# Performance work log

Hardware: AMD Instinct MI355X
Metric: run time of the kernel (lower is better)

## Reference

```python
import jax, jax.numpy as jnp
import numpy as np

N_STATE = 64   # S4 state size N
L_MAX = 4096   # sequence length
H = 256        # number of SSM channels (d_model)
BATCH = 16


def _green_roots(Lambda, P, B, C, step, L):
    """Frequency-domain S4 kernel at the L roots of unity (Q = P, DPLR).
    Lambda,P,B,C: complex[N]; step: scalar. Returns complex[L]."""
    Omega = jnp.exp(-2j * jnp.pi * (jnp.arange(L) / L))          # (L,)
    g = (2.0 / step) * ((1.0 - Omega) / (1.0 + Omega))           # (L,)
    c = 2.0 / (1.0 + Omega)                                      # (L,)
    # four Cauchy numerators stacked: k00,k01,k10,k11
    vs = jnp.stack([C.conj() * B, C.conj() * P,
                    P.conj() * B, P.conj() * P])                 # (4,N)
    denom = g[:, None] - Lambda[None, :]                         # (L,N)
    k = jnp.einsum('kn,ln->kl', vs, 1.0 / denom)                 # (4,L)
    k00, k01, k10, k11 = k
    return c * (k00 - k01 * (1.0 / (1.0 + k11)) * k10)           # (L,)


def _kernel_freq(Lambda_re, Lambda_im, P_re, P_im, B_re, B_im,
                 C_re, C_im, log_step, L):
    Lambda = (Lambda_re + 1j * Lambda_im).astype(jnp.complex64)  # (H,N)
    P = (P_re + 1j * P_im).astype(jnp.complex64)
    Bm = (B_re + 1j * B_im).astype(jnp.complex64)
    Cm = (C_re + 1j * C_im).astype(jnp.complex64)
    step = jnp.exp(log_step)                                     # (H,)
    f = lambda lam, p, b, c, s: _green_roots(lam, p, b, c, s, L)
    return jax.vmap(f)(Lambda, P, Bm, Cm, step)                  # (H,L)


def setup_inputs() -> dict:
    key = jax.random.key(0)
    ks = jax.random.split(key, 10)
    u = jax.random.normal(ks[0], (BATCH, H, L_MAX), dtype=jnp.float32)
    # stable continuous-time poles: negative real part, spread imag parts
    Lambda_re = -0.5 * jnp.ones((H, N_STATE), jnp.float32) \
        - jax.random.uniform(ks[1], (H, N_STATE), dtype=jnp.float32)
    Lambda_im = jnp.pi * jax.random.normal(ks[2], (H, N_STATE), dtype=jnp.float32) * N_STATE / 8
    scale = 1.0 / np.sqrt(N_STATE)
    P_re = scale * jax.random.normal(ks[3], (H, N_STATE), dtype=jnp.float32)
    P_im = scale * jax.random.normal(ks[4], (H, N_STATE), dtype=jnp.float32)
    B_re = scale * jax.random.normal(ks[5], (H, N_STATE), dtype=jnp.float32)
    B_im = scale * jax.random.normal(ks[6], (H, N_STATE), dtype=jnp.float32)
    C_re = scale * jax.random.normal(ks[7], (H, N_STATE), dtype=jnp.float32)
    C_im = scale * jax.random.normal(ks[8], (H, N_STATE), dtype=jnp.float32)
    # log-uniform step in [1e-3, 1e-1] (log_step_initializer)
    log_step = (jax.random.uniform(ks[9], (H,), dtype=jnp.float32)
                * (np.log(0.1) - np.log(0.001)) + np.log(0.001)).astype(jnp.float32)
    return {"u": u, "Lambda_re": Lambda_re, "Lambda_im": Lambda_im,
            "P_re": P_re, "P_im": P_im, "B_re": B_re, "B_im": B_im,
            "C_re": C_re, "C_im": C_im, "log_step": log_step}


def reference(u, Lambda_re, Lambda_im, P_re, P_im, B_re, B_im,
              C_re, C_im, log_step):
    L = u.shape[-1]
    Kf = _kernel_freq(Lambda_re, Lambda_im, P_re, P_im, B_re, B_im,
                      C_re, C_im, log_step, L)                   # (H,L) complex
    # circular_convolution_complex, batched over (BATCH,H)
    ud = jnp.fft.fft(u, axis=-1)                                  # (B,H,L)
    y = jnp.fft.ifft(ud * Kf[None, :, :], n=L, axis=-1)
    return y.real.astype(jnp.float32)                             # (B,H,L)
```

## Files before the change

### kernel.cpp

```cpp
#include <hip/hip_runtime.h>
#include <math.h>

#define NSTATE 64
#define LEN    4096
#define NH     256
#define NB     16

__device__ float2 g_ksym[NH * LEN];
__device__ float4 g_pA[NH * NSTATE];
__device__ float4 g_pB[NH * NSTATE];
__device__ float2 g_pC[NH * NSTATE];

__device__ __forceinline__ int rev8_12(int p) {
  return ((p & 7) << 9) | (((p >> 3) & 7) << 6) | (((p >> 6) & 7) << 3) | (p >> 9);
}

__device__ __forceinline__ float2 cadd(float2 a, float2 b){ return make_float2(a.x+b.x, a.y+b.y); }
__device__ __forceinline__ float2 csub(float2 a, float2 b){ return make_float2(a.x-b.x, a.y-b.y); }
__device__ __forceinline__ float2 cmul(float2 a, float2 b){ return make_float2(a.x*b.x - a.y*b.y, a.x*b.y + a.y*b.x); }
__device__ __forceinline__ float2 mulnegi(float2 a){ return make_float2(a.y, -a.x); }
__device__ __forceinline__ float2 mulposi(float2 a){ return make_float2(-a.y, a.x); }

#define RSQ2 0.70710678118654752f

__device__ __forceinline__ void bfly8_fwd(float2 v[8]) {
  float2 a0 = cadd(v[0], v[4]), b0 = csub(v[0], v[4]);
  float2 a1 = cadd(v[1], v[5]), d1 = csub(v[1], v[5]);
  float2 a2 = cadd(v[2], v[6]), d2 = csub(v[2], v[6]);
  float2 a3 = cadd(v[3], v[7]), d3 = csub(v[3], v[7]);
  float2 b1 = make_float2(RSQ2 * (d1.x + d1.y), RSQ2 * (d1.y - d1.x));
  float2 b2 = mulnegi(d2);
  float2 b3 = make_float2(RSQ2 * (d3.y - d3.x), -RSQ2 * (d3.x + d3.y));
  float2 u0 = cadd(a0, a2), u1 = csub(a0, a2), u2 = cadd(a1, a3), u3 = csub(a1, a3);
  v[0] = cadd(u0, u2);
  v[2] = cadd(u1, mulnegi(u3));
  v[4] = csub(u0, u2);
  v[6] = cadd(u1, mulposi(u3));
  float2 w0 = cadd(b0, b2), w1 = csub(b0, b2), w2 = cadd(b1, b3), w3 = csub(b1, b3);
  v[1] = cadd(w0, w2);
  v[3] = cadd(w1, mulnegi(w3));
  v[5] = csub(w0, w2);
  v[7] = cadd(w1, mulposi(w3));
}

__device__ __forceinline__ void bfly8_inv(float2 v[8]) {
  float2 a0 = cadd(v[0], v[4]), b0 = csub(v[0], v[4]);
  float2 a1 = cadd(v[1], v[5]), d1 = csub(v[1], v[5]);
  float2 a2 = cadd(v[2], v[6]), d2 = csub(v[2], v[6]);
  float2 a3 = cadd(v[3], v[7]), d3 = csub(v[3], v[7]);
  float2 b1 = make_float2(RSQ2 * (d1.x - d1.y), RSQ2 * (d1.x + d1.y));
  float2 b2 = mulposi(d2);
  float2 b3 = make_float2(-RSQ2 * (d3.x + d3.y), RSQ2 * (d3.x - d3.y));
  float2 u0 = cadd(a0, a2), u1 = csub(a0, a2), u2 = cadd(a1, a3), u3 = csub(a1, a3);
  v[0] = cadd(u0, u2);
  v[2] = cadd(u1, mulposi(u3));
  v[4] = csub(u0, u2);
  v[6] = cadd(u1, mulnegi(u3));
  float2 w0 = cadd(b0, b2), w1 = csub(b0, b2), w2 = cadd(b1, b3), w3 = csub(b1, b3);
  v[1] = cadd(w0, w2);
  v[3] = cadd(w1, mulposi(w3));
  v[5] = csub(w0, w2);
  v[7] = cadd(w1, mulnegi(w3));
}

__device__ __forceinline__ void twiddle7(float2 v[8], float wr, float wi) {
  float2 w1 = make_float2(wr, wi);
  float2 w2 = cmul(w1, w1);
  float2 w3 = cmul(w2, w1);
  float2 w4 = cmul(w2, w2);
  float2 w5 = cmul(w3, w2);
  float2 w6 = cmul(w3, w3);
  float2 w7 = cmul(w4, w3);
  v[1] = cmul(v[1], w1); v[2] = cmul(v[2], w2); v[3] = cmul(v[3], w3);
  v[4] = cmul(v[4], w4); v[5] = cmul(v[5], w5); v[6] = cmul(v[6], w6);
  v[7] = cmul(v[7], w7);
}

#define WAVE_SYNC() asm volatile("s_waitcnt lgkmcnt(0)" ::: "memory")

__global__ __launch_bounds__(256) void s4_prep(
    const float* __restrict__ Lre, const float* __restrict__ Lim,
    const float* __restrict__ Pre, const float* __restrict__ Pim,
    const float* __restrict__ Bre, const float* __restrict__ Bim,
    const float* __restrict__ Cre, const float* __restrict__ Cim)
{
  int idx = blockIdx.x * 256 + threadIdx.x;
  if (idx >= NH * NSTATE) return;
  float lr = Lre[idx], li = Lim[idx];
  float pr = Pre[idx], pi = Pim[idx];
  float br = Bre[idx], bi = Bim[idx];
  float cr = Cre[idx], ci = Cim[idx];
  g_pA[idx] = make_float4(lr, li, pr * pr + pi * pi, 0.0f);
  g_pB[idx] = make_float4(cr * br + ci * bi, cr * bi - ci * br,
                          cr * pr + ci * pi, cr * pi - ci * pr);
  g_pC[idx] = make_float2(pr * br + pi * bi, pr * bi - pi * br);
}

__global__ __launch_bounds__(256) void s4_kernel_freq(const float* __restrict__ log_step)
{
  const int b = blockIdx.x;
  const int h = b >> 2;
  const int q = ((b & 3) << 8) | threadIdx.x;
  const float step = expf(log_step[h]);
  const float ts = 2.0f / step;
  const float NEG2PI = -6.2831853071795864769f;

  float gar, gai, car, cai, gbr, gbi, cbr, cbi;
  float gcr, gci, ccr, cci, gdr, gdi, cdr, cdi;
  {
    float so, co;
    sincosf(NEG2PI * ((float)q * (1.0f / (float)LEN)), &so, &co);
    float dr = 1.0f + co, di = so;
    float inv = 1.0f / fmaf(dr, dr, di * di);
    car = 2.0f * dr * inv; cai = -2.0f * di * inv;
    float nr = 1.0f - co, ni = -so;
    gar = ts * (fmaf(nr, dr, ni * di) * inv);
    gai = ts * (fmaf(ni, dr, -nr * di) * inv);
  }
  if (q == 0) {
    float so, co;
    sincosf(NEG2PI * 0.5f, &so, &co);
    float dr = 1.0f + co, di = so;
    float inv = 1.0f / fmaf(dr, dr, di * di);
    cbr = 2.0f * dr * inv; cbi = -2.0f * di * inv;
    float nr = 1.0f - co, ni = -so;
    gbr = ts * (fmaf(nr, dr, ni * di) * inv);
    gbi = ts * (fmaf(ni, dr, -nr * di) * inv);
  } else {
    gbr = gar; gbi = -gai; cbr = car; cbi = -cai;
  }
  {
    float so, co;
    sincosf(NEG2PI * ((float)(q + 1024) * (1.0f / (float)LEN)), &so, &co);
    float dr = 1.0f + co, di = so;
    float inv = 1.0f / fmaf(dr, dr, di * di);
    ccr = 2.0f * dr * inv; cci = -2.0f * di * inv;
    float nr = 1.0f - co, ni = -so;
    gcr = ts * (fmaf(nr, dr, ni * di) * inv);
    gci = ts * (fmaf(ni, dr, -nr * di) * inv);
  }
  gdr = gcr; gdi = -gci; cdr = ccr; cdi = -cci;

  float A00r=0,A00i=0,A01r=0,A01i=0,A10r=0,A10i=0,A11r=0,A11i=0;
  float B00r=0,B00i=0,B01r=0,B01i=0,B10r=0,B10i=0,B11r=0,B11i=0;
  float C00r=0,C00i=0,C01r=0,C01i=0,C10r=0,C10i=0,C11r=0,C11i=0;
  float D00r=0,D00i=0,D01r=0,D01i=0,D10r=0,D10i=0,D11r=0,D11i=0;

  const float4* __restrict__ pa = g_pA + h * NSTATE;
  const float4* __restrict__ pb = g_pB + h * NSTATE;
  const float2* __restrict__ pc = g_pC + h * NSTATE;

#define CAUCHY(gre, gim, k00r,k00i,k01r,k01i,k10r,k10i,k11r,k11i)            \
  {                                                                          \
    float rd = gre - Av.x, id = gim - Av.y;                                  \
    float idn = __builtin_amdgcn_rcpf(fmaf(rd, rd, id * id));                \
    float ir = rd * idn, ii = -(id * idn);                                   \
    k00r = fmaf(Bv.x, ir, k00r); k00r = fmaf(-Bv.y, ii, k00r);               \
    k00i = fmaf(Bv.x, ii, k00i); k00i = fmaf(Bv.y, ir, k00i);                \
    k01r = fmaf(Bv.z, ir, k01r); k01r = fmaf(-Bv.w, ii, k01r);               \
    k01i = fmaf(Bv.z, ii, k01i); k01i = fmaf(Bv.w, ir, k01i);                \
    k10r = fmaf(Cv.x, ir, k10r); k10r = fmaf(-Cv.y, ii, k10r);               \
    k10i = fmaf(Cv.x, ii, k10i); k10i = fmaf(Cv.y, ir, k10i);                \
    k11r = fmaf(Av.z, ir, k11r); k11i = fmaf(Av.z, ii, k11i);                \
  }

#pragma unroll 4
  for (int n = 0; n < NSTATE; ++n) {
    float4 Av = pa[n];
    float4 Bv = pb[n];
    float2 Cv = pc[n];
    CAUCHY(gar, gai, A00r,A00i,A01r,A01i,A10r,A10i,A11r,A11i)
    CAUCHY(gbr, gbi, B00r,B00i,B01r,B01i,B10r,B10i,B11r,B11i)
    CAUCHY(gcr, gci, C00r,C00i,C01r,C01i,C10r,C10i,C11r,C11i)
    CAUCHY(gdr, gdi, D00r,D00i,D01r,D01i,D10r,D10i,D11r,D11i)
  }
#undef CAUCHY

#define FINISH(cr_, ci_, k00r,k00i,k01r,k01i,k10r,k10i,k11r,k11i, Kr, Ki)    \
  {                                                                          \
    float rr = 1.0f + k11r, ri = k11i;                                       \
    float rinv = 1.0f / fmaf(rr, rr, ri * ri);                               \
    float pr_ = k01r * k10r - k01i * k10i;                                   \
    float pi_ = k01r * k10i + k01i * k10r;                                   \
    float wr = (pr_ * rr + pi_ * ri) * rinv;                                 \
    float wi = (pi_ * rr - pr_ * ri) * rinv;                                 \
    float sr = k00r - wr, si = k00i - wi;                                    \
    Kr = cr_ * sr - ci_ * si; Ki = cr_ * si + ci_ * sr;                      \
  }

  float Kar, Kai, Kbr, Kbi, Kcr, Kci, Kdr, Kdi;
  FINISH(car, cai, A00r,A00i,A01r,A01i,A10r,A10i,A11r,A11i, Kar, Kai)
  FINISH(cbr, cbi, B00r,B00i,B01r,B01i,B10r,B10i,B11r,B11i, Kbr, Kbi)
  FINISH(ccr, cci, C00r,C00i,C01r,C01i,C10r,C10i,C11r,C11i, Kcr, Kci)
  FINISH(cdr, cdi, D00r,D00i,D01r,D01i,D10r,D10i,D11r,D11i, Kdr, Kdi)
#undef FINISH

  float2* out = g_ksym + (size_t)h * LEN;
  if (q == 0) {
    out[rev8_12(0)]    = make_float2(Kar, 0.0f);
    out[rev8_12(2048)] = make_float2(Kbr, 0.0f);
  } else {
    float fr = 0.5f * (Kar + Kbr), fi = 0.5f * (Kai - Kbi);
    out[rev8_12(q)]       = make_float2(fr, fi);
    out[rev8_12(LEN - q)] = make_float2(fr, -fi);
  }
  {
    float fr = 0.5f * (Kcr + Kdr), fi = 0.5f * (Kci - Kdi);
    out[rev8_12(1024 + q)] = make_float2(fr, fi);
    out[rev8_12(3072 - q)] = make_float2(fr, -fi);
  }
}

__global__ __launch_bounds__(512) void s4_fftconv(const float* __restrict__ u,
                                                 float* __restrict__ y)
{
  __shared__ float2 X[4608];

  const int t = threadIdx.x;
  const int bid = blockIdx.x;
  const int h  = bid & (NH - 1);
  const int bp = bid >> 8;

  const int w  = t >> 6;
  const int i  = t & 63;
  const int i3 = i >> 3;
  const int i7 = i & 7;
  const int R  = 576 * w;

  float c1, s1, c2, s2, c3, s3;
  sincosf((float)t  * (-6.2831853071795864769f / 4096.0f), &s1, &c1);
  sincosf((float)i  * (-6.2831853071795864769f /  512.0f), &s2, &c2);
  sincosf((float)i7 * (-6.2831853071795864769f /   64.0f), &s3, &c3);

  const float* u1 = u + ((size_t)bp * NH + h) * LEN;
  const float* u2 = u + ((size_t)(bp + 8) * NH + h) * LEN;

  float2 v[8];
#pragma unroll
  for (int m = 0; m < 8; ++m)
    v[m] = make_float2(u1[t + 512 * m], u2[t + 512 * m]);
  bfly8_fwd(v);
  twiddle7(v, c1, s1);
#pragma unroll
  for (int m = 0; m < 8; ++m) X[576 * m + t] = v[m];
  __syncthreads();

#pragma unroll
  for (int m = 0; m < 8; ++m) v[m] = X[R + i + 64 * m];
  bfly8_fwd(v);
  twiddle7(v, c2, s2);
#pragma unroll
  for (int m = 0; m < 8; ++m) X[R + 68 * m + i] = v[m];
  WAVE_SYNC();

#pragma unroll
  for (int m = 0; m < 8; ++m) v[m] = X[R + 68 * i3 + i7 + 8 * m];
  bfly8_fwd(v);
  twiddle7(v, c3, s3);
#pragma unroll
  for (int m = 0; m < 8; ++m) X[R + 9 * (8 * i3 + m) + i7] = v[m];
  WAVE_SYNC();

  {
    const float4* kp = (const float4*)(g_ksym + (size_t)h * LEN + 8 * t);
    float4 k0 = kp[0], k1 = kp[1], k2 = kp[2], k3 = kp[3];
#pragma unroll
    for (int m = 0; m < 8; ++m) v[m] = X[R + 9 * i + m];
    bfly8_fwd(v);
    v[0] = cmul(v[0], make_float2(k0.x, k0.y));
    v[1] = cmul(v[1], make_float2(k0.z, k0.w));
    v[2] = cmul(v[2], make_float2(k1.x, k1.y));
    v[3] = cmul(v[3], make_float2(k1.z, k1.w));
    v[4] = cmul(v[4], make_float2(k2.x, k2.y));
    v[5] = cmul(v[5], make_float2(k2.z, k2.w));
    v[6] = cmul(v[6], make_float2(k3.x, k3.y));
    v[7] = cmul(v[7], make_float2(k3.z, k3.w));
    bfly8_inv(v);
#pragma unroll
    for (int p = 0; p < 8; ++p) X[R + 9 * i + p] = v[p];
  }
  WAVE_SYNC();

#pragma unroll
  for (int m = 0; m < 8; ++m) v[m] = X[R + 9 * (8 * i3 + m) + i7];
  twiddle7(v, c3, -s3);
  bfly8_inv(v);
#pragma unroll
  for (int p = 0; p < 8; ++p) X[R + 68 * i3 + i7 + 8 * p] = v[p];
  WAVE_SYNC();

#pragma unroll
  for (int m = 0; m < 8; ++m) v[m] = X[R + 68 * m + i];
  twiddle7(v, c2, -s2);
  bfly8_inv(v);
#pragma unroll
  for (int p = 0; p < 8; ++p) X[R + i + 64 * p] = v[p];
  __syncthreads();

#pragma unroll
  for (int m = 0; m < 8; ++m) v[m] = X[576 * m + t];
  twiddle7(v, c1, -s1);
  bfly8_inv(v);

  float* y1 = y + ((size_t)bp * NH + h) * LEN;
  float* y2 = y + ((size_t)(bp + 8) * NH + h) * LEN;
  const float sc = 1.0f / (float)LEN;
#pragma unroll
  for (int p = 0; p < 8; ++p) {
    y1[t + 512 * p] = v[p].x * sc;
    y2[t + 512 * p] = v[p].y * sc;
  }
}

extern "C" void kernel_launch(void* const* d_in, const int* in_sizes, int n_in,
                              void* d_out, int out_size, void* d_ws, size_t ws_size,
                              hipStream_t stream) {
  const float* u    = (const float*)d_in[0];
  const float* Lre  = (const float*)d_in[1];
  const float* Lim  = (const float*)d_in[2];
  const float* Pre  = (const float*)d_in[3];
  const float* Pim  = (const float*)d_in[4];
  const float* Bre  = (const float*)d_in[5];
  const float* Bim  = (const float*)d_in[6];
  const float* Cre  = (const float*)d_in[7];
  const float* Cim  = (const float*)d_in[8];
  const float* lstep = (const float*)d_in[9];
  float* y = (float*)d_out;

  s4_prep<<<(NH * NSTATE + 255) / 256, 256, 0, stream>>>(Lre, Lim, Pre, Pim, Bre, Bim, Cre, Cim);
  s4_kernel_freq<<<NH * 4, 256, 0, stream>>>(lstep);
  s4_fftconv<<<NH * (NB / 2), 512, 0, stream>>>(u, y);
}
```

Baseline: 180.4 us.

## Fuse S4 prep into kernel-frequency kernel with shared-memory parameters and more blocks

Removes the separate prep kernel and computes the per-channel Cauchy numerators inside the frequency kernel, storing them in shared memory instead of global scratch arrays. Each thread now evaluates two conjugate frequency points instead of four, and the grid is doubled to NH*8 blocks, lowering register pressure and raising parallelism. The intent is to save one kernel launch and the global round trip. The cost is redundant prep work: each of the 8 blocks per channel recomputes the same 64 parameters, plus an added block barrier.

```diff
diff --git a/kernel.cpp b/kernel.cpp
--- a/kernel.cpp
+++ b/kernel.cpp
@@ -7,9 +7,6 @@
 #define NB     16
 
 __device__ float2 g_ksym[NH * LEN];
-__device__ float4 g_pA[NH * NSTATE];
-__device__ float4 g_pB[NH * NSTATE];
-__device__ float2 g_pC[NH * NSTATE];
 
 __device__ __forceinline__ int rev8_12(int p) {
   return ((p & 7) << 9) | (((p >> 3) & 7) << 6) | (((p >> 6) & 7) << 3) | (p >> 9);
@@ -78,38 +75,41 @@
 
 #define WAVE_SYNC() asm volatile("s_waitcnt lgkmcnt(0)" ::: "memory")
 
-__global__ __launch_bounds__(256) void s4_prep(
+__global__ __launch_bounds__(256) void s4_kernel_freq(
     const float* __restrict__ Lre, const float* __restrict__ Lim,
     const float* __restrict__ Pre, const float* __restrict__ Pim,
     const float* __restrict__ Bre, const float* __restrict__ Bim,
-    const float* __restrict__ Cre, const float* __restrict__ Cim)
+    const float* __restrict__ Cre, const float* __restrict__ Cim,
+    const float* __restrict__ log_step)
 {
-  int idx = blockIdx.x * 256 + threadIdx.x;
-  if (idx >= NH * NSTATE) return;
-  float lr = Lre[idx], li = Lim[idx];
-  float pr = Pre[idx], pi = Pim[idx];
-  float br = Bre[idx], bi = Bim[idx];
-  float cr = Cre[idx], ci = Cim[idx];
-  g_pA[idx] = make_float4(lr, li, pr * pr + pi * pi, 0.0f);
-  g_pB[idx] = make_float4(cr * br + ci * bi, cr * bi - ci * br,
-                          cr * pr + ci * pi, cr * pi - ci * pr);
-  g_pC[idx] = make_float2(pr * br + pi * bi, pr * bi - pi * br);
-}
-
-__global__ __launch_bounds__(256) void s4_kernel_freq(const float* __restrict__ log_step)
-{
-  const int b = blockIdx.x;
-  const int h = b >> 2;
-  const int q = ((b & 3) << 8) | threadIdx.x;
+  __shared__ float4 sA[NSTATE];
+  __shared__ float4 sB[NSTATE];
+  __shared__ float2 sC[NSTATE];
+
+  const int blk = blockIdx.x;
+  const int h = blk >> 3;
+  const int j = ((blk & 7) << 8) | threadIdx.x;
+
+  if (threadIdx.x < NSTATE) {
+    int idx = h * NSTATE + threadIdx.x;
+    float lr = Lre[idx], li = Lim[idx];
+    float pr = Pre[idx], pi = Pim[idx];
+    float br = Bre[idx], bi = Bim[idx];
+    float cr = Cre[idx], ci = Cim[idx];
+    sA[threadIdx.x] = make_float4(lr, li, pr * pr + pi * pi, 0.0f);
+    sB[threadIdx.x] = make_float4(cr * br + ci * bi, cr * bi - ci * br,
+                                  cr * pr + ci * pi, cr * pi - ci * pr);
+    sC[threadIdx.x] = make_float2(pr * br + pi * bi, pr * bi - pi * br);
+  }
+
   const float step = expf(log_step[h]);
   const float ts = 2.0f / step;
   const float NEG2PI = -6.2831853071795864769f;
 
   float gar, gai, car, cai, gbr, gbi, cbr, cbi;
-  float gcr, gci, ccr, cci, gdr, gdi, cdr, cdi;
   {
     float so, co;
-    sincosf(NEG2PI * ((float)q * (1.0f / (float)LEN)), &so, &co);
+    sincosf(NEG2PI * ((float)j * (1.0f / (float)LEN)), &so, &co);
     float dr = 1.0f + co, di = so;
     float inv = 1.0f / fmaf(dr, dr, di * di);
     car = 2.0f * dr * inv; cai = -2.0f * di * inv;
@@ -117,7 +117,7 @@
     gar = ts * (fmaf(nr, dr, ni * di) * inv);
     gai = ts * (fmaf(ni, dr, -nr * di) * inv);
   }
-  if (q == 0) {
+  if (j == 0) {
     float so, co;
     sincosf(NEG2PI * 0.5f, &so, &co);
     float dr = 1.0f + co, di = so;
@@ -129,26 +129,11 @@
   } else {
     gbr = gar; gbi = -gai; cbr = car; cbi = -cai;
   }
-  {
-    float so, co;
-    sincosf(NEG2PI * ((float)(q + 1024) * (1.0f / (float)LEN)), &so, &co);
-    float dr = 1.0f + co, di = so;
-    float inv = 1.0f / fmaf(dr, dr, di * di);
-    ccr = 2.0f * dr * inv; cci = -2.0f * di * inv;
-    float nr = 1.0f - co, ni = -so;
-    gcr = ts * (fmaf(nr, dr, ni * di) * inv);
-    gci = ts * (fmaf(ni, dr, -nr * di) * inv);
-  }
-  gdr = gcr; gdi = -gci; cdr = ccr; cdi = -cci;
 
   float A00r=0,A00i=0,A01r=0,A01i=0,A10r=0,A10i=0,A11r=0,A11i=0;
   float B00r=0,B00i=0,B01r=0,B01i=0,B10r=0,B10i=0,B11r=0,B11i=0;
-  float C00r=0,C00i=0,C01r=0,C01i=0,C10r=0,C10i=0,C11r=0,C11i=0;
-  float D00r=0,D00i=0,D01r=0,D01i=0,D10r=0,D10i=0,D11r=0,D11i=0;
-
-  const float4* __restrict__ pa = g_pA + h * NSTATE;
-  const float4* __restrict__ pb = g_pB + h * NSTATE;
-  const float2* __restrict__ pc = g_pC + h * NSTATE;
+
+  __syncthreads();
 
 #define CAUCHY(gre, gim, k00r,k00i,k01r,k01i,k10r,k10i,k11r,k11i)            \
   {                                                                          \
@@ -164,15 +149,13 @@
     k11r = fmaf(Av.z, ir, k11r); k11i = fmaf(Av.z, ii, k11i);                \
   }
 
-#pragma unroll 4
+#pragma unroll 8
   for (int n = 0; n < NSTATE; ++n) {
-    float4 Av = pa[n];
-    float4 Bv = pb[n];
-    float2 Cv = pc[n];
+    float4 Av = sA[n];
+    float4 Bv = sB[n];
+    float2 Cv = sC[n];
     CAUCHY(gar, gai, A00r,A00i,A01r,A01i,A10r,A10i,A11r,A11i)
     CAUCHY(gbr, gbi, B00r,B00i,B01r,B01i,B10r,B10i,B11r,B11i)
-    CAUCHY(gcr, gci, C00r,C00i,C01r,C01i,C10r,C10i,C11r,C11i)
-    CAUCHY(gdr, gdi, D00r,D00i,D01r,D01i,D10r,D10i,D11r,D11i)
   }
 #undef CAUCHY
 
@@ -188,26 +171,19 @@
     Kr = cr_ * sr - ci_ * si; Ki = cr_ * si + ci_ * sr;                      \
   }
 
-  float Kar, Kai, Kbr, Kbi, Kcr, Kci, Kdr, Kdi;
+  float Kar, Kai, Kbr, Kbi;
   FINISH(car, cai, A00r,A00i,A01r,A01i,A10r,A10i,A11r,A11i, Kar, Kai)
   FINISH(cbr, cbi, B00r,B00i,B01r,B01i,B10r,B10i,B11r,B11i, Kbr, Kbi)
-  FINISH(ccr, cci, C00r,C00i,C01r,C01i,C10r,C10i,C11r,C11i, Kcr, Kci)
-  FINISH(cdr, cdi, D00r,D00i,D01r,D01i,D10r,D10i,D11r,D11i, Kdr, Kdi)
 #undef FINISH
 
   float2* out = g_ksym + (size_t)h * LEN;
-  if (q == 0) {
+  if (j == 0) {
     out[rev8_12(0)]    = make_float2(Kar, 0.0f);
     out[rev8_12(2048)] = make_float2(Kbr, 0.0f);
   } else {
     float fr = 0.5f * (Kar + Kbr), fi = 0.5f * (Kai - Kbi);
-    out[rev8_12(q)]       = make_float2(fr, fi);
-    out[rev8_12(LEN - q)] = make_float2(fr, -fi);
-  }
-  {
-    float fr = 0.5f * (Kcr + Kdr), fi = 0.5f * (Kci - Kdi);
-    out[rev8_12(1024 + q)] = make_float2(fr, fi);
-    out[rev8_12(3072 - q)] = make_float2(fr, -fi);
+    out[rev8_12(j)]       = make_float2(fr, fi);
+    out[rev8_12(LEN - j)] = make_float2(fr, -fi);
   }
 }
 
@@ -327,7 +303,6 @@
   const float* lstep = (const float*)d_in[9];
   float* y = (float*)d_out;
 
-  s4_prep<<<(NH * NSTATE + 255) / 256, 256, 0, stream>>>(Lre, Lim, Pre, Pim, Bre, Bim, Cre, Cim);
-  s4_kernel_freq<<<NH * 4, 256, 0, stream>>>(lstep);
+  s4_kernel_freq<<<NH * 8, 256, 0, stream>>>(Lre, Lim, Pre, Pim, Bre, Bim, Cre, Cim, lstep);
   s4_fftconv<<<NH * (NB / 2), 512, 0, stream>>>(u, y);
 }
```

After: 180.3 us. About the same (-0.1%).
